# Optimization experiments

Hardware: AMD Instinct MI355X
Metric: run time of the kernel (lower is better)

The kernel has to match this reference:

```python
import jax, jax.numpy as jnp
import numpy as np
from jax import lax

DN = ('NCDHW', 'OIDHW', 'NCDHW')  # dimension numbers matching torch Conv3d (cross-correlation)


def setup_inputs() -> dict:
    key = jax.random.key(0)
    k0, k1, k2, k3 = jax.random.split(key, 4)
    B, P, C = 32, 2048, 512
    x = jax.random.normal(k0, (B, P, C), dtype=jnp.float32)
    w1 = jax.random.normal(k1, (1, 1, 1, 1, 1), dtype=jnp.float32)
    w2 = jax.random.normal(k2, (1, 1, 2, 2, 2), dtype=jnp.float32)
    w3 = jax.random.normal(k3, (1, 1, 3, 3, 3), dtype=jnp.float32)
    return {"x": x, "w1": w1, "w2": w2, "w3": w3}


def reference(x, w1, w2, w3):
    B, P, C = x.shape
    t = P // 16
    # [B,P,C] -> [B,C,t,4,4]
    xv = jnp.transpose(x, (0, 2, 1)).reshape(B, C, t, 4, 4)
    # x_shift: [B,t,C,4,4] -> [B*t, C, 4, 4]
    x_shift = jnp.transpose(xv, (0, 2, 1, 3, 4)).reshape(B * t, C, 4, 4)
    # channel mean -> [B,1,t,4,4]
    xm = jnp.mean(xv, axis=1, keepdims=True)
    # ST_1: 1x1x1 conv, no pad
    p1 = lax.conv_general_dilated(xm, w1, (1, 1, 1), 'VALID', dimension_numbers=DN)
    # ST_2: pad (left=1 on t,h,w), then 2x2x2 valid conv -> same shape
    xp = jnp.pad(xm, ((0, 0), (0, 0), (1, 0), (1, 0), (1, 0)))
    p2 = lax.conv_general_dilated(xp, w2, (1, 1, 1), 'VALID', dimension_numbers=DN)
    # ST_3: 3x3x3 conv with padding 1 -> same shape
    p3 = lax.conv_general_dilated(xm, w3, (1, 1, 1), [(1, 1), (1, 1), (1, 1)], dimension_numbers=DN)
    g = p1 + p2 + p3  # [B,1,t,4,4]
    # transpose(2,1) -> [B,t,1,4,4] -> [B*t,1,4,4]
    g = jnp.transpose(g, (0, 2, 1, 3, 4)).reshape(B * t, 1, 4, 4)
    out = x_shift * jax.nn.sigmoid(g)  # broadcast over C
    # back to [B,P,C]
    out = out.reshape(B, t, C, 4, 4)
    out = jnp.transpose(out, (0, 2, 1, 3, 4)).reshape(B, C, P)
    return jnp.transpose(out, (0, 2, 1))
```

## Files before the change

kernel.cpp:

```cpp
#include <hip/hip_runtime.h>
#include <math.h>

#define BB 32
#define PP 2048
#define CC 512
#define TT 128
#define NROWS (BB*PP)

__global__ __launch_bounds__(256) void row_mean_kernel(
        const float* __restrict__ x, float* __restrict__ mean) {
    int wave = threadIdx.x >> 6;
    int lane = threadIdx.x & 63;
    int row  = blockIdx.x * 4 + wave;
    const float4* xr = (const float4*)(x + (size_t)row * CC);
    float4 a = xr[lane];
    float4 b = xr[lane + 64];
    float s = (a.x + a.y) + (a.z + a.w) + (b.x + b.y) + (b.z + b.w);
    #pragma unroll
    for (int off = 32; off > 0; off >>= 1)
        s += __shfl_down(s, off, 64);
    if (lane == 0) mean[row] = s * (1.0f / 512.0f);
}

__global__ __launch_bounds__(256) void gate_kernel(
        const float* __restrict__ mean,
        const float* __restrict__ w1, const float* __restrict__ w2,
        const float* __restrict__ w3, float* __restrict__ gate) {
    int r = blockIdx.x * blockDim.x + threadIdx.x;
    if (r >= NROWS) return;
    int b = r >> 11;
    int p = r & 2047;
    int t = p >> 4;
    int h = (p >> 2) & 3;
    int w = p & 3;
    const float* mb = mean + ((size_t)b << 11);
    float g = 0.0f;
    #pragma unroll
    for (int i = 0; i < 3; ++i) {
        int tt = t + i - 1;
        if (tt < 0 || tt >= TT) continue;
        #pragma unroll
        for (int j = 0; j < 3; ++j) {
            int hh = h + j - 1;
            if (hh < 0 || hh >= 4) continue;
            #pragma unroll
            for (int k = 0; k < 3; ++k) {
                int ww = w + k - 1;
                if (ww < 0 || ww >= 4) continue;
                float wt = w3[i * 9 + j * 3 + k];
                if (i < 2 && j < 2 && k < 2) wt += w2[i * 4 + j * 2 + k];
                if (i == 1 && j == 1 && k == 1) wt += w1[0];
                g += wt * mb[tt * 16 + hh * 4 + ww];
            }
        }
    }
    gate[r] = 1.0f / (1.0f + __expf(-g));
}

__global__ __launch_bounds__(256) void scale_kernel(
        const float* __restrict__ x, const float* __restrict__ gate,
        float* __restrict__ out) {
    size_t q = (size_t)blockIdx.x * blockDim.x + threadIdx.x;
    int r = (int)(q >> 7);
    float s = gate[r];
    float4 v = ((const float4*)x)[q];
    v.x *= s; v.y *= s; v.z *= s; v.w *= s;
    ((float4*)out)[q] = v;
}

extern "C" void kernel_launch(void* const* d_in, const int* in_sizes, int n_in,
                              void* d_out, int out_size, void* d_ws, size_t ws_size,
                              hipStream_t stream) {
    const float* x  = (const float*)d_in[0];
    const float* w1 = (const float*)d_in[1];
    const float* w2 = (const float*)d_in[2];
    const float* w3 = (const float*)d_in[3];
    float* out  = (float*)d_out;
    float* mean = (float*)d_ws;
    float* gate = mean + NROWS;

    row_mean_kernel<<<NROWS / 4, 256, 0, stream>>>(x, mean);
    gate_kernel<<<NROWS / 256, 256, 0, stream>>>(mean, w1, w2, w3, gate);
    scale_kernel<<<(NROWS * (CC / 4)) / 256, 256, 0, stream>>>(x, gate, out);
}
```

Baseline: 248.7 us.

## Fuse row-mean, gate stencil and scaling into one tiled kernel

```diff
diff --git a/kernel.cpp b/kernel.cpp
--- a/kernel.cpp
+++ b/kernel.cpp
@@ -5,67 +5,86 @@
 #define PP 2048
 #define CC 512
 #define TT 128
-#define NROWS (BB*PP)
+#define TB 16
+#define HALO_ROWS ((TB + 2) * 16)
+#define OWN_ROWS  (TB * 16)
 
-__global__ __launch_bounds__(256) void row_mean_kernel(
-        const float* __restrict__ x, float* __restrict__ mean) {
+typedef float f4_t __attribute__((ext_vector_type(4)));
+
+__global__ __launch_bounds__(1024) void fused_kernel(
+        const float* __restrict__ x,
+        const float* __restrict__ w1, const float* __restrict__ w2,
+        const float* __restrict__ w3, float* __restrict__ out) {
+    __shared__ float lmean[HALO_ROWS];
+    __shared__ float lgate[OWN_ROWS];
+
+    int blk  = blockIdx.x;
+    int b    = blk >> 3;
+    int t0   = (blk & 7) * TB;
     int wave = threadIdx.x >> 6;
     int lane = threadIdx.x & 63;
-    int row  = blockIdx.x * 4 + wave;
-    const float4* xr = (const float4*)(x + (size_t)row * CC);
-    float4 a = xr[lane];
-    float4 b = xr[lane + 64];
-    float s = (a.x + a.y) + (a.z + a.w) + (b.x + b.y) + (b.z + b.w);
+    const size_t xbase = (size_t)b * (PP * CC);
+
     #pragma unroll
-    for (int off = 32; off > 0; off >>= 1)
-        s += __shfl_down(s, off, 64);
-    if (lane == 0) mean[row] = s * (1.0f / 512.0f);
-}
+    for (int rr = 0; rr < 18; ++rr) {
+        int r = wave * 18 + rr;
+        int t = t0 - 1 + (r >> 4);
+        if (t < 0 || t >= TT) continue;
+        int p = t * 16 + (r & 15);
+        const float4* xr = (const float4*)(x + xbase + (size_t)p * CC);
+        float4 va = xr[lane];
+        float4 vb = xr[lane + 64];
+        float s = (va.x + va.y) + (va.z + va.w) + (vb.x + vb.y) + (vb.z + vb.w);
+        #pragma unroll
+        for (int off = 32; off; off >>= 1) s += __shfl_down(s, off, 64);
+        if (lane == 0) lmean[r] = s * (1.0f / 512.0f);
+    }
+    __syncthreads();
 
-__global__ __launch_bounds__(256) void gate_kernel(
-        const float* __restrict__ mean,
-        const float* __restrict__ w1, const float* __restrict__ w2,
-        const float* __restrict__ w3, float* __restrict__ gate) {
-    int r = blockIdx.x * blockDim.x + threadIdx.x;
-    if (r >= NROWS) return;
-    int b = r >> 11;
-    int p = r & 2047;
-    int t = p >> 4;
-    int h = (p >> 2) & 3;
-    int w = p & 3;
-    const float* mb = mean + ((size_t)b << 11);
-    float g = 0.0f;
-    #pragma unroll
-    for (int i = 0; i < 3; ++i) {
-        int tt = t + i - 1;
-        if (tt < 0 || tt >= TT) continue;
+    if (threadIdx.x < OWN_ROWS) {
+        int i  = threadIdx.x;
+        int tl = i >> 4;
+        int h  = (i >> 2) & 3;
+        int w  = i & 3;
+        int tg = t0 + tl;
+        float g = 0.0f;
         #pragma unroll
-        for (int j = 0; j < 3; ++j) {
-            int hh = h + j - 1;
-            if (hh < 0 || hh >= 4) continue;
+        for (int ii = 0; ii < 3; ++ii) {
+            int tt = tg + ii - 1;
+            if (tt < 0 || tt >= TT) continue;
             #pragma unroll
-            for (int k = 0; k < 3; ++k) {
-                int ww = w + k - 1;
-                if (ww < 0 || ww >= 4) continue;
-                float wt = w3[i * 9 + j * 3 + k];
-                if (i < 2 && j < 2 && k < 2) wt += w2[i * 4 + j * 2 + k];
-                if (i == 1 && j == 1 && k == 1) wt += w1[0];
-                g += wt * mb[tt * 16 + hh * 4 + ww];
+            for (int jj = 0; jj < 3; ++jj) {
+                int hh = h + jj - 1;
+                if (hh < 0 || hh >= 4) continue;
+                #pragma unroll
+                for (int kk = 0; kk < 3; ++kk) {
+                    int ww = w + kk - 1;
+                    if (ww < 0 || ww >= 4) continue;
+                    float wt = w3[ii * 9 + jj * 3 + kk];
+                    if (ii < 2 && jj < 2 && kk < 2) wt += w2[ii * 4 + jj * 2 + kk];
+                    if (ii == 1 && jj == 1 && kk == 1) wt += w1[0];
+                    g += wt * lmean[(tl + ii) * 16 + hh * 4 + ww];
+                }
             }
         }
+        lgate[i] = 1.0f / (1.0f + __expf(-g));
     }
-    gate[r] = 1.0f / (1.0f + __expf(-g));
-}
+    __syncthreads();
 
-__global__ __launch_bounds__(256) void scale_kernel(
-        const float* __restrict__ x, const float* __restrict__ gate,
-        float* __restrict__ out) {
-    size_t q = (size_t)blockIdx.x * blockDim.x + threadIdx.x;
-    int r = (int)(q >> 7);
-    float s = gate[r];
-    float4 v = ((const float4*)x)[q];
-    v.x *= s; v.y *= s; v.z *= s; v.w *= s;
-    ((float4*)out)[q] = v;
+    #pragma unroll
+    for (int rr = 0; rr < 16; ++rr) {
+        int i = wave * 16 + rr;
+        int p = t0 * 16 + i;
+        float gg = lgate[i];
+        const float4* xr = (const float4*)(x + xbase + (size_t)p * CC);
+        f4_t* orow = (f4_t*)(out + xbase + (size_t)p * CC);
+        float4 va = xr[lane];
+        float4 vb = xr[lane + 64];
+        f4_t ra = { va.x * gg, va.y * gg, va.z * gg, va.w * gg };
+        f4_t rb = { vb.x * gg, vb.y * gg, vb.z * gg, vb.w * gg };
+        __builtin_nontemporal_store(ra, &orow[lane]);
+        __builtin_nontemporal_store(rb, &orow[lane + 64]);
+    }
 }
 
 extern "C" void kernel_launch(void* const* d_in, const int* in_sizes, int n_in,
@@ -75,11 +94,7 @@
     const float* w1 = (const float*)d_in[1];
     const float* w2 = (const float*)d_in[2];
     const float* w3 = (const float*)d_in[3];
-    float* out  = (float*)d_out;
-    float* mean = (float*)d_ws;
-    float* gate = mean + NROWS;
+    float* out = (float*)d_out;
 
-    row_mean_kernel<<<NROWS / 4, 256, 0, stream>>>(x, mean);
-    gate_kernel<<<NROWS / 256, 256, 0, stream>>>(mean, w1, w2, w3, gate);
-    scale_kernel<<<(NROWS * (CC / 4)) / 256, 256, 0, stream>>>(x, gate, out);
+    fused_kernel<<<BB * (TT / TB), 1024, 0, stream>>>(x, w1, w2, w3, out);
 }
```

Measured after the change: 254.2 us. +2.2%, slower.
